# Kernel optimization log

Hardware: AMD Instinct MI355X
Metric: run time of the kernel (lower is better)

The kernel has to match this reference:

```python
import jax, jax.numpy as jnp
import numpy as np

DG = 8            # deformable_groups
MAX_RES = 10.0    # max_residual_magnitude
K = 9             # 3x3 kernel positions


def conv3(x, w, b):
    y = jax.lax.conv_general_dilated(x, w, (1, 1), [(1, 1), (1, 1)],
                                     dimension_numbers=('NCHW', 'OIHW', 'NCHW'))
    return y + b[None, :, None, None]


def lrelu(v):
    return jnp.where(v >= 0, v, 0.1 * v)


def deform_conv2d(x, offset, mask, weight, bias):
    # x: [B,C,H,W]; offset: [B,2*DG*K,H,W] (per group, K points, (y,x) interleaved)
    # mask: [B,DG*K,H,W]; weight: [O,C,3,3]; stride=1, pad=1, dil=1, groups=1
    B, C, H, W = x.shape
    Cg = C // DG
    off = offset.reshape(B, DG, K, 2, H, W)
    dtype = x.dtype
    dy = (jnp.arange(K) // 3 - 1).astype(dtype)
    dx = (jnp.arange(K) % 3 - 1).astype(dtype)
    py = off[:, :, :, 0] + jnp.arange(H, dtype=dtype)[None, None, None, :, None] + dy[None, None, :, None, None]
    px = off[:, :, :, 1] + jnp.arange(W, dtype=dtype)[None, None, None, None, :] + dx[None, None, :, None, None]
    y0 = jnp.floor(py)
    x0 = jnp.floor(px)
    x_flat = x.reshape(B, DG, Cg, H * W)
    m = mask.reshape(B, DG, K, H, W)
    acc = jnp.zeros((B, DG, Cg, K, H, W), dtype=dtype)
    for iy, wy in ((y0, y0 + 1.0 - py), (y0 + 1.0, py - y0)):
        for ix, wx in ((x0, x0 + 1.0 - px), (x0 + 1.0, px - x0)):
            valid = (iy >= 0) & (iy < H) & (ix >= 0) & (ix < W)
            yi = jnp.clip(iy, 0, H - 1).astype(jnp.int32)
            xi = jnp.clip(ix, 0, W - 1).astype(jnp.int32)
            idx = (yi * W + xi).reshape(B, DG, 1, K * H * W)
            g = jnp.take_along_axis(x_flat, idx, axis=3).reshape(B, DG, Cg, K, H, W)
            wgt = (wy * wx * valid.astype(dtype) * m)[:, :, None]  # mask folded in
            acc = acc + g * wgt
    O = weight.shape[0]
    out = jnp.einsum('bgckhw,ogck->bohw', acc, weight.reshape(O, DG, Cg, K))
    return out + bias[None, :, None, None]


def setup_inputs() -> dict:
    key = jax.random.key(0)
    ks = jax.random.split(key, 12)
    B, C, H, W = 4, 64, 128, 128
    inp = {
        'x': jax.random.normal(ks[0], (B, C, H, W), jnp.float32),
        'x_warped0': jax.random.normal(ks[1], (B, C, H, W), jnp.float32),
        'x_current': jax.random.normal(ks[2], (B, C, H, W), jnp.float32),
        'flow0': jax.random.normal(ks[3], (B, 2, H, W), jnp.float32),
        'w1': jax.random.normal(ks[4], (64, 130, 3, 3), jnp.float32) * 0.05,
        'b1': jnp.zeros((64,), jnp.float32),
        'w2': jax.random.normal(ks[5], (64, 64, 3, 3), jnp.float32) * 0.05,
        'b2': jnp.zeros((64,), jnp.float32),
        'w3': jax.random.normal(ks[6], (64, 64, 3, 3), jnp.float32) * 0.05,
        'b3': jnp.zeros((64,), jnp.float32),
        'w4': jax.random.normal(ks[7], (216, 64, 3, 3), jnp.float32) * 0.05,
        'b4': jnp.zeros((216,), jnp.float32),
        'weight': jax.random.normal(ks[8], (64, 64, 3, 3), jnp.float32) * 0.05,
        'bias': jnp.zeros((64,), jnp.float32),
    }
    return inp


def reference(x, x_warped0, x_current, flow0, w1, b1, w2, b2, w3, b3, w4, b4, weight, bias):
    # conv_offset stack on cat([x_warped0, x_current, flow0])
    feat = jnp.concatenate([x_warped0, x_current, flow0], axis=1)  # [B, 2C+2, H, W]
    o = lrelu(conv3(feat, w1, b1))
    o = lrelu(conv3(o, w2, b2))
    o = lrelu(conv3(o, w3, b3))
    o = conv3(o, w4, b4)  # [B, 3*K*DG, H, W]
    out1, out2, mask = jnp.split(o, 3, axis=1)
    offset = MAX_RES * jnp.tanh(jnp.concatenate([out1, out2], axis=1))  # [B, 2*K*DG, H, W]
    # flows[0].flip(1).repeat(1, K*DG, 1, 1): (y,x) flow tiled over all sample points
    offset = offset + jnp.tile(flow0[:, ::-1], (1, K * DG, 1, 1))
    mask = jax.nn.sigmoid(mask)
    return deform_conv2d(x, offset, mask, weight, bias)
```

## Files before the change

### kernel.cpp

```cpp
#include <hip/hip_runtime.h>
#include <math.h>

#define HH 128
#define WW 128
#define BB 4
#define HW (HH*WW)

typedef unsigned short u16;
typedef unsigned int u32;
typedef __bf16 bf16x8 __attribute__((ext_vector_type(8)));
typedef float f32x4 __attribute__((ext_vector_type(4)));

__device__ __forceinline__ u16 f2bf(float x) {
    u32 u = __float_as_uint(x);
    return (u16)((u + 0x7fffu + ((u >> 16) & 1u)) >> 16);
}
__device__ __forceinline__ float bf2f(u16 h) {
    return __uint_as_float(((u32)h) << 16);
}
__device__ __forceinline__ bf16x8 ld8(const u16* p) {
    union { uint4 u; bf16x8 v; } c;
    c.u = *(const uint4*)p;
    return c.v;
}
__device__ __forceinline__ bf16x8 cvt8(uint4 u) {
    union { uint4 u; bf16x8 v; } c;
    c.u = u;
    return c.v;
}

__global__ void split_w_k(const float* __restrict__ src, u16* __restrict__ dh,
                          u16* __restrict__ dl, int OC, int OCpad, int CIN, int CINpad)
{
    const int i = blockIdx.x * 256 + threadIdx.x;
    const int tot = OCpad * 9 * CINpad;
    if (i >= tot) return;
    const int oc = i / (9 * CINpad);
    const int r = i - oc * 9 * CINpad;
    const int tap = r / CINpad;
    const int cin = r - tap * CINpad;
    float v = 0.f;
    if (oc < OC && cin < CIN) v = src[((size_t)oc * CIN + cin) * 9 + tap];
    const u16 h = f2bf(v);
    dh[i] = h;
    dl[i] = f2bf(v - bf2f(h));
}

__global__ void pad_bias_k(const float* __restrict__ b, float* __restrict__ bp)
{
    const int i = blockIdx.x * 256 + threadIdx.x;
    if (i < 256) bp[i] = (i < 216) ? b[i] : 0.f;
}

__global__ void pack_dw_k(const float* __restrict__ wt, u16* __restrict__ Apack)
{
    const int i = blockIdx.x * 256 + threadIdx.x;
    if (i >= 36864) return;
    const int jj = i & 7;
    const int fr = (i >> 3) & 15;
    const int m  = (i >> 7) & 3;
    const int fq = (i >> 9) & 3;
    const int kk = i >> 11;
    const int oc = m * 16 + fr;
    const int j  = kk * 32 + fq * 8 + jj;
    const int tap = j >> 3, c = j & 7;
    const int g = tap / 9, kt = tap - g * 9;
    const int ch = g * 8 + c;
    Apack[i] = f2bf(wt[((size_t)oc * 64 + ch) * 9 + kt]);
}

template<int CREC>
__global__ __launch_bounds__(256) void pack_x_k(
    const float* __restrict__ A, const float* __restrict__ B2,
    const float* __restrict__ C3, u16* __restrict__ dst)
{
    const int i = blockIdx.x * 256 + threadIdx.x;
    const int b = i >> 14;
    const int px = i & 16383;
    u16* rec = dst + (size_t)i * (CREC * 2);

#pragma unroll
    for (int g = 0; g < CREC / 32; ++g) {
#pragma unroll
        for (int cb = 0; cb < 4; ++cb) {
            u32 hwv[4], lwv[4];
#pragma unroll
            for (int p = 0; p < 4; ++p) {
                float v[2];
#pragma unroll
                for (int e = 0; e < 2; ++e) {
                    const int c = g * 32 + cb * 8 + p * 2 + e;
                    float vv;
                    if (c < 64)       vv = A[((size_t)(b * 64 + c)) * HW + px];
                    else if (c < 128) vv = B2[((size_t)(b * 64 + c - 64)) * HW + px];
                    else if (c < 130) vv = C3[((size_t)(b * 2 + c - 128)) * HW + px];
                    else              vv = 0.f;
                    v[e] = vv;
                }
                const u16 h0 = f2bf(v[0]), h1 = f2bf(v[1]);
                const u16 l0 = f2bf(v[0] - bf2f(h0)), l1 = f2bf(v[1] - bf2f(h1));
                hwv[p] = (u32)h0 | ((u32)h1 << 16);
                lwv[p] = (u32)l0 | ((u32)l1 << 16);
            }
            uint4 H; H.x = hwv[0]; H.y = hwv[1]; H.z = hwv[2]; H.w = hwv[3];
            uint4 L; L.x = lwv[0]; L.y = lwv[1]; L.z = lwv[2]; L.w = lwv[3];
            *(uint4*)(rec + g * 64 + cb * 16)     = H;
            *(uint4*)(rec + g * 64 + cb * 16 + 8) = L;
        }
    }
}

template<int NCHUNK, int KGLAST, int MODE, bool RELU, bool PACKOUT, int MINW, int NJ>
__global__ __launch_bounds__(256, MINW) void conv_pk_k(
    const u16* __restrict__ Xp, const u16* __restrict__ Wh, const u16* __restrict__ Wl,
    const float* __restrict__ bias, float* __restrict__ outf, u16* __restrict__ outp,
    int OCreal)
{
    const int ROWS = 4;
    const int NPX = (ROWS + 2) * 18;
    __shared__ u16 Xs[NPX * 136];
    const int CINpad = (NCHUNK - 1) * 64 + KGLAST * 32;
    const int CRECU16 = CINpad * 2;

    const int tile = blockIdx.x;
    const int h0 = (tile >> 3) * ROWS;
    const int w0 = (tile & 7) * 16;
    const int b = blockIdx.z;
    const int t = threadIdx.x;
    const int lane = t & 63, wv = t >> 6;
    const int fr = lane & 15, fq = lane >> 4;

    const int mbase = (MODE == 1) ? (wv * NJ) : 0;

    f32x4 acc0[4];
    f32x4 acc1[NJ][4];
    if (MODE == 0) {
        const float4 bv = *(const float4*)(bias + wv * 16 + 4 * fq);
#pragma unroll
        for (int n = 0; n < 4; ++n) {
            acc0[n][0] = bv.x; acc0[n][1] = bv.y; acc0[n][2] = bv.z; acc0[n][3] = bv.w;
        }
    } else {
#pragma unroll
        for (int m = 0; m < NJ; ++m) {
            const float4 bv = *(const float4*)(bias + (mbase + m) * 16 + 4 * fq);
#pragma unroll
            for (int n = 0; n < 4; ++n) {
                acc1[m][n][0] = bv.x; acc1[m][n][1] = bv.y;
                acc1[m][n][2] = bv.z; acc1[m][n][3] = bv.w;
            }
        }
    }

    const u16* WhL = Wh + (size_t)fr * 9 * CINpad + 8 * fq;
    const u16* WlL = Wl + (size_t)fr * 9 * CINpad + 8 * fq;

#pragma unroll
    for (int chunk = 0; chunk < NCHUNK; ++chunk) {
        const int nkg = (chunk == NCHUNK - 1) ? KGLAST : 2;
        const int nu = nkg * 8;
        __syncthreads();
        for (int s = t; s < NPX * nu; s += 256) {
            const int px = s / nu, o = s - px * nu;
            const int hy = px / 18, hx = px - hy * 18;
            const int gy = h0 + hy - 1, gx = w0 + hx - 1;
            uint4 v; v.x = 0; v.y = 0; v.z = 0; v.w = 0;
            if (gy >= 0 && gy < HH && gx >= 0 && gx < WW)
                v = *(const uint4*)(Xp + ((size_t)(b * HW + gy * WW + gx)) * CRECU16
                                       + chunk * 128 + o * 8);
            *(uint4*)(Xs + px * 136 + o * 8) = v;
        }
        __syncthreads();

        if (MODE == 0) {
#pragma unroll
            for (int tap = 0; tap < 9; ++tap) {
                const int ky = tap / 3, kx = tap % 3;
#pragma unroll
                for (int kg = 0; kg < 2; ++kg) {
                    if (kg >= nkg) break;
                    const size_t off = (size_t)(wv * 144 + tap) * CINpad + chunk * 64 + kg * 32;
                    const bf16x8 Ah = ld8(WhL + off);
                    const bf16x8 Al = ld8(WlL + off);
#pragma unroll
                    for (int n = 0; n < 4; ++n) {
                        const int hp = (n + ky) * 18 + fr + kx;
                        const u16* Bp = Xs + hp * 136 + kg * 64 + fq * 16;
                        const bf16x8 Bh = ld8(Bp);
                        const bf16x8 Bl = ld8(Bp + 8);
                        acc0[n] = __builtin_amdgcn_mfma_f32_16x16x32_bf16(Ah, Bh, acc0[n], 0, 0, 0);
                        acc0[n] = __builtin_amdgcn_mfma_f32_16x16x32_bf16(Ah, Bl, acc0[n], 0, 0, 0);
                        acc0[n] = __builtin_amdgcn_mfma_f32_16x16x32_bf16(Al, Bh, acc0[n], 0, 0, 0);
                    }
                }
            }
        } else {
            auto PF = [&](int tap, bf16x8 (&Dh)[2 * NJ], bf16x8 (&Dl)[2 * NJ]) {
#pragma unroll
                for (int kg = 0; kg < 2; ++kg)
#pragma unroll
                    for (int m = 0; m < NJ; ++m) {
                        const size_t off = (size_t)((mbase + m) * 144 + tap) * CINpad
                                         + chunk * 64 + kg * 32;
                        Dh[kg * NJ + m] = ld8(WhL + off);
                        Dl[kg * NJ + m] = ld8(WlL + off);
                    }
            };
            auto CMP = [&](int tap, bf16x8 (&Dh)[2 * NJ], bf16x8 (&Dl)[2 * NJ]) {
                const int ky = tap / 3, kx = tap - 3 * ky;
#pragma unroll
                for (int kg = 0; kg < 2; ++kg) {
#pragma unroll
                    for (int n = 0; n < 4; ++n) {
                        const int hp = (n + ky) * 18 + fr + kx;
                        const u16* Bp = Xs + hp * 136 + kg * 64 + fq * 16;
                        const bf16x8 Bh = ld8(Bp);
                        const bf16x8 Bl = ld8(Bp + 8);
#pragma unroll
                        for (int m = 0; m < NJ; ++m) {
                            acc1[m][n] = __builtin_amdgcn_mfma_f32_16x16x32_bf16(Dh[kg * NJ + m], Bh, acc1[m][n], 0, 0, 0);
                            acc1[m][n] = __builtin_amdgcn_mfma_f32_16x16x32_bf16(Dh[kg * NJ + m], Bl, acc1[m][n], 0, 0, 0);
                            acc1[m][n] = __builtin_amdgcn_mfma_f32_16x16x32_bf16(Dl[kg * NJ + m], Bh, acc1[m][n], 0, 0, 0);
                        }
                    }
                }
            };

            bf16x8 PaH[2 * NJ], PaL[2 * NJ], PbH[2 * NJ], PbL[2 * NJ];
            PF(0, PaH, PaL);
#pragma unroll 1
            for (int tp = 0; tp < 4; ++tp) {
                PF(2 * tp + 1, PbH, PbL);
                CMP(2 * tp, PaH, PaL);
                PF(2 * tp + 2, PaH, PaL);
                CMP(2 * tp + 1, PbH, PbL);
            }
            CMP(8, PaH, PaL);
        }
    }

    if (MODE == 1) {
#pragma unroll
        for (int m = 0; m < NJ; ++m) {
            const int mt = mbase + m;
#pragma unroll
            for (int n = 0; n < 4; ++n)
#pragma unroll
                for (int i = 0; i < 4; ++i) {
                    const int oc = mt * 16 + 4 * fq + i;
                    if (oc < OCreal) {
                        float v = acc1[m][n][i];
                        if (mt < 9) {
                            const float a = fabsf(v);
                            const float e = __expf(-2.f * a);
                            float tv = (1.f - e) * __builtin_amdgcn_rcpf(1.f + e);
                            v = 10.f * copysignf(tv, v);
                        } else {
                            v = __builtin_amdgcn_rcpf(1.f + __expf(-v));
                        }
                        outf[((size_t)(b * OCreal + oc)) * HW + (h0 + n) * WW + w0 + fr] = v;
                    }
                }
        }
    } else if (!PACKOUT) {
#pragma unroll
        for (int n = 0; n < 4; ++n)
#pragma unroll
            for (int i = 0; i < 4; ++i) {
                const int oc = wv * 16 + 4 * fq + i;
                if (oc < OCreal) {
                    float v = acc0[n][i];
                    if (RELU) v = (v >= 0.f) ? v : 0.1f * v;
                    outf[((size_t)(b * OCreal + oc)) * HW + (h0 + n) * WW + w0 + fr] = v;
                }
            }
    } else {
        __syncthreads();
        const int coff = (wv >> 1) * 64 + (((wv << 1) + (fq >> 1)) & 3) * 16 + ((fq & 1) << 2);
#pragma unroll
        for (int n = 0; n < 4; ++n) {
            u16 hh[4], ll[4];
#pragma unroll
            for (int i = 0; i < 4; ++i) {
                float v = acc0[n][i];
                if (RELU) v = (v >= 0.f) ? v : 0.1f * v;
                hh[i] = f2bf(v);
                ll[i] = f2bf(v - bf2f(hh[i]));
            }
            uint2 H, L;
            H.x = (u32)hh[0] | ((u32)hh[1] << 16);
            H.y = (u32)hh[2] | ((u32)hh[3] << 16);
            L.x = (u32)ll[0] | ((u32)ll[1] << 16);
            L.y = (u32)ll[2] | ((u32)ll[3] << 16);
            const int pxe = n * 16 + fr;
            u16* E = Xs + pxe * 136 + coff;
            *(uint2*)E = H;
            *(uint2*)(E + 8) = L;
        }
        __syncthreads();
        for (int i = t; i < 1024; i += 256) {
            const int px = i >> 4, o = i & 15;
            const uint4 v = *(const uint4*)(Xs + px * 136 + o * 8);
            const int gp = (h0 + (px >> 4)) * WW + w0 + (px & 15);
            *(uint4*)(outp + ((size_t)(b * HW + gp)) * 128 + o * 8) = v;
        }
    }
}

__global__ __launch_bounds__(256) void pack_xb_k(
    const float* __restrict__ x, uint4* __restrict__ xqb)
{
    const int i = blockIdx.x * 256 + threadIdx.x;
    const int pix = i & (HW - 1);
    const int g = (i >> 14) & 7;
    const int b = i >> 17;
    const float* xp = x + ((size_t)(b * 64 + g * 8)) * HW + pix;
    u32 w[4];
#pragma unroll
    for (int c2 = 0; c2 < 4; ++c2) {
        const u16 l = f2bf(xp[(size_t)(2 * c2) * HW]);
        const u16 h = f2bf(xp[(size_t)(2 * c2 + 1) * HW]);
        w[c2] = (u32)l | ((u32)h << 16);
    }
    uint4 v; v.x = w[0]; v.y = w[1]; v.z = w[2]; v.w = w[3];
    xqb[(size_t)(b * 8 + g) * HW + pix] = v;
}

__device__ __forceinline__ unsigned pk_bf16(float lo, float hi) {
    unsigned a = __float_as_uint(lo), b = __float_as_uint(hi);
    return ((a + 0x8000u) >> 16) | ((b + 0x8000u) & 0xffff0000u);
}

__global__ __launch_bounds__(512, 8) void deform_fused_k(
    const uint4* __restrict__ xqb, const float* __restrict__ o4,
    const float* __restrict__ flow, const uint4* __restrict__ Apack,
    const float* __restrict__ bias, float* __restrict__ out)
{
    __shared__ u16 sv[32 * 584];

    const int bid0 = blockIdx.x;
    const int bid = (bid0 & 7) * 256 + (bid0 >> 3);
    const int b = bid >> 9;
    const int pix0 = (bid & 511) << 5;
    const int t = threadIdx.x;

    {
        const int gpx = t & 31;
        const int g = (t >> 5) & 7;
        const int kh = t >> 8;
        const int kbase = kh * 4;
        const int pix = pix0 + gpx;
        const int h = pix >> 7, w = pix & (WW - 1);
        const float fy = flow[((size_t)b * 2 + 1) * HW + pix];
        const float fx = flow[((size_t)b * 2 + 0) * HW + pix];
        const float* ob = o4 + (size_t)b * 216 * HW + pix;
        const uint4* qg = xqb + (size_t)(b * 8 + g) * HW;

        int   code[5];
        float w00[5], w01[5], w10[5], w11[5];

#pragma unroll
        for (int j = 0; j < 5; ++j) {
            if (j == 4 && !kh) break;
            const int k = kbase + j;
            const float oy = ob[(size_t)(g * 18 + k * 2) * HW];
            const float ox = ob[(size_t)(g * 18 + k * 2 + 1) * HW];
            const float mm = ob[(size_t)(144 + g * 9 + k) * HW];

            const float ppy = oy + fy + (float)(h + k / 3 - 1);
            const float ppx = ox + fx + (float)(w + k % 3 - 1);

            const float y0f = floorf(ppy), x0f = floorf(ppx);
            const float ly = ppy - y0f, lx = ppx - x0f;
            const int iy0 = (int)y0f, ix0 = (int)x0f;
            const int iy1 = iy0 + 1,  ix1 = ix0 + 1;

            const float vy0 = (iy0 >= 0 && iy0 < HH) ? 1.f : 0.f;
            const float vy1 = (iy1 >= 0 && iy1 < HH) ? 1.f : 0.f;
            const float vx0 = (ix0 >= 0 && ix0 < WW) ? 1.f : 0.f;
            const float vx1 = (ix1 >= 0 && ix1 < WW) ? 1.f : 0.f;

            const int cy0 = min(max(iy0, 0), HH - 1);
            const int cy1 = min(max(iy1, 0), HH - 1);
            const int cx0 = min(max(ix0, 0), WW - 1);
            const int cx1 = min(max(ix1, 0), WW - 1);

            w00[j] = (1.f - ly) * (1.f - lx) * vy0 * vx0 * mm;
            w01[j] = (1.f - ly) * lx         * vy0 * vx1 * mm;
            w10[j] = ly         * (1.f - lx) * vy1 * vx0 * mm;
            w11[j] = ly         * lx         * vy1 * vx1 * mm;

            code[j] = (cy0 * WW + cx0) | ((cx1 - cx0) << 14) | ((cy1 - cy0) << 15);
        }

        u16* svp = sv + gpx * 584 + g * 72 + kbase * 8;
#pragma unroll
        for (int j = 0; j < 5; ++j) {
            if (j == 4 && !kh) break;
            const int i00 = code[j] & 16383;
            const int i01 = i00 + ((code[j] >> 14) & 1);
            const int i10 = i00 + (((code[j] >> 15) & 1) << 7);
            const int i11 = i10 + ((code[j] >> 14) & 1);

            const uint4 A4 = qg[i00];
            const uint4 B4 = qg[i01];
            const uint4 C4 = qg[i10];
            const uint4 D4 = qg[i11];
            const float W00 = w00[j], W01 = w01[j], W10 = w10[j], W11 = w11[j];

            uint4 P;
            u32 pw[4];
#pragma unroll
            for (int c2 = 0; c2 < 4; ++c2) {
                const u32 aw = (&A4.x)[c2], bw = (&B4.x)[c2];
                const u32 cw = (&C4.x)[c2], dw = (&D4.x)[c2];
                const float alo = __uint_as_float(aw << 16), ahi = __uint_as_float(aw & 0xffff0000u);
                const float blo = __uint_as_float(bw << 16), bhi = __uint_as_float(bw & 0xffff0000u);
                const float clo = __uint_as_float(cw << 16), chi = __uint_as_float(cw & 0xffff0000u);
                const float dlo = __uint_as_float(dw << 16), dhi = __uint_as_float(dw & 0xffff0000u);
                const float slo = W00 * alo + W01 * blo + W10 * clo + W11 * dlo;
                const float shi = W00 * ahi + W01 * bhi + W10 * chi + W11 * dhi;
                pw[c2] = pk_bf16(slo, shi);
            }
            P.x = pw[0]; P.y = pw[1]; P.z = pw[2]; P.w = pw[3];
            *(uint4*)(svp + (size_t)j * 8) = P;
        }
    }
    __syncthreads();

    {
        const int lane = t & 63, wv = t >> 6;
        const int mt = wv & 3, nt = wv >> 2;
        const int fr = lane & 15, fq = lane >> 4;

        f32x4 acc;
        acc[0] = 0.f; acc[1] = 0.f; acc[2] = 0.f; acc[3] = 0.f;

#pragma unroll
        for (int kk = 0; kk < 18; ++kk) {
            const bf16x8 A = cvt8(Apack[((kk * 4 + fq) * 4 + mt) * 16 + fr]);
            const bf16x8 Bf = ld8(sv + (size_t)(nt * 16 + fr) * 584 + kk * 32 + fq * 8);
            acc = __builtin_amdgcn_mfma_f32_16x16x32_bf16(A, Bf, acc, 0, 0, 0);
        }

        const float4 bv = *(const float4*)(bias + mt * 16 + 4 * fq);
        const float bb[4] = { bv.x, bv.y, bv.z, bv.w };
        const int pix = pix0 + nt * 16 + fr;
#pragma unroll
        for (int i = 0; i < 4; ++i) {
            const int oc = mt * 16 + 4 * fq + i;
            out[((size_t)b * 64 + oc) * HW + pix] = acc[i] + bb[i];
        }
    }
}

extern "C" void kernel_launch(void* const* d_in, const int* in_sizes, int n_in,
                              void* d_out, int out_size, void* d_ws, size_t ws_size,
                              hipStream_t stream)
{
    const float* x     = (const float*)d_in[0];
    const float* xw    = (const float*)d_in[1];
    const float* xc    = (const float*)d_in[2];
    const float* flow  = (const float*)d_in[3];
    const float* w1    = (const float*)d_in[4];
    const float* b1    = (const float*)d_in[5];
    const float* w2    = (const float*)d_in[6];
    const float* b2    = (const float*)d_in[7];
    const float* w3    = (const float*)d_in[8];
    const float* b3    = (const float*)d_in[9];
    const float* w4    = (const float*)d_in[10];
    const float* b4    = (const float*)d_in[11];
    const float* wt    = (const float*)d_in[12];
    const float* bias  = (const float*)d_in[13];
    float* out = (float*)d_out;

    char* ws = (char*)d_ws;
    u16*   X1p  = (u16*)(ws);
    float* o4   = (float*)(ws);
    u16*   buf1 = (u16*)(ws + 56623104);
    u16*   buf2 = (u16*)(ws + 73400320);
    u16* Apack = (u16*)(ws + 90177536);
    u16* W1h = (u16*)(ws + 90251264);
    u16* W1l = (u16*)(ws + 90435584);
    u16* W2h = (u16*)(ws + 90619904);
    u16* W2l = (u16*)(ws + 90693632);
    u16* W3h = (u16*)(ws + 90767360);
    u16* W3l = (u16*)(ws + 90841088);
    u16* W4h = (u16*)(ws + 90914816);
    u16* W4l = (u16*)(ws + 91209728);
    float* b4p = (float*)(ws + 91504640);

    const dim3 blk(256);

    split_w_k<<<dim3((64 * 9 * 160 + 255) / 256), blk, 0, stream>>>(w1, W1h, W1l, 64, 64, 130, 160);
    split_w_k<<<dim3((64 * 9 * 64 + 255) / 256), blk, 0, stream>>>(w2, W2h, W2l, 64, 64, 64, 64);
    split_w_k<<<dim3((64 * 9 * 64 + 255) / 256), blk, 0, stream>>>(w3, W3h, W3l, 64, 64, 64, 64);
    split_w_k<<<dim3((256 * 9 * 64 + 255) / 256), blk, 0, stream>>>(w4, W4h, W4l, 216, 256, 64, 64);
    pad_bias_k<<<dim3(1), blk, 0, stream>>>(b4, b4p);
    pack_dw_k<<<dim3(144), blk, 0, stream>>>(wt, Apack);

    pack_x_k<160><<<dim3(BB * HW / 256), blk, 0, stream>>>(xw, xc, flow, X1p);
    conv_pk_k<3, 1, 0, true, true, 2, 4><<<dim3(256, 1, BB), blk, 0, stream>>>(
        X1p, W1h, W1l, b1, nullptr, buf1, 64);
    conv_pk_k<1, 2, 0, true, true, 2, 4><<<dim3(256, 1, BB), blk, 0, stream>>>(
        buf1, W2h, W2l, b2, nullptr, buf2, 64);
    conv_pk_k<1, 2, 0, true, true, 2, 4><<<dim3(256, 1, BB), blk, 0, stream>>>(
        buf2, W3h, W3l, b3, nullptr, buf1, 64);
    pack_xb_k<<<dim3(BB * 8 * HW / 256), blk, 0, stream>>>(x, (uint4*)buf2);
    conv_pk_k<1, 2, 1, false, false, 1, 4><<<dim3(256, 1, BB), blk, 0, stream>>>(
        buf1, W4h, W4l, b4p, o4, nullptr, 216);

    deform_fused_k<<<dim3(BB * HW / 32), dim3(512), 0, stream>>>(
        (const uint4*)buf2, o4, flow, (const uint4*)Apack, bias, out);
}
```

Measured before the change: 285.4 us.

## Retile offset/mask conv into 8-row tiles split across channel halves

```diff
diff --git a/kernel.cpp b/kernel.cpp
--- a/kernel.cpp
+++ b/kernel.cpp
@@ -116,7 +116,7 @@
     const float* __restrict__ bias, float* __restrict__ outf, u16* __restrict__ outp,
     int OCreal)
 {
-    const int ROWS = 4;
+    const int ROWS = (MODE == 1) ? 8 : 4;
     const int NPX = (ROWS + 2) * 18;
     __shared__ u16 Xs[NPX * 136];
     const int CINpad = (NCHUNK - 1) * 64 + KGLAST * 32;
@@ -130,7 +130,8 @@
     const int lane = t & 63, wv = t >> 6;
     const int fr = lane & 15, fq = lane >> 4;
 
-    const int mbase = (MODE == 1) ? (wv * NJ) : 0;
+    const int mg = wv >> 1, rg = wv & 1;
+    const int mbase = (MODE == 1) ? (blockIdx.y * 8 + mg * NJ) : 0;
 
     f32x4 acc0[4];
     f32x4 acc1[NJ][4];
@@ -195,47 +196,46 @@
                 }
             }
         } else {
-            auto PF = [&](int tap, bf16x8 (&Dh)[2 * NJ], bf16x8 (&Dl)[2 * NJ]) {
-#pragma unroll
-                for (int kg = 0; kg < 2; ++kg)
+            auto PF = [&](int s, bf16x8 (&Dh)[NJ], bf16x8 (&Dl)[NJ]) {
+                const int tap = s >> 1, kg = s & 1;
+#pragma unroll
+                for (int m = 0; m < NJ; ++m) {
+                    const size_t off = (size_t)((mbase + m) * 144 + tap) * CINpad
+                                     + chunk * 64 + kg * 32;
+                    Dh[m] = ld8(WhL + off);
+                    Dl[m] = ld8(WlL + off);
+                }
+            };
+            auto CMP = [&](int s, bf16x8 (&Dh)[NJ], bf16x8 (&Dl)[NJ]) {
+                const int tap = s >> 1, kg = s & 1;
+                const int ky = tap / 3, kx = tap - 3 * ky;
+#pragma unroll
+                for (int n = 0; n < 4; ++n) {
+                    const int hp = (rg * 4 + n + ky) * 18 + fr + kx;
+                    const u16* Bp = Xs + hp * 136 + kg * 64 + fq * 16;
+                    const bf16x8 Bh = ld8(Bp);
+                    const bf16x8 Bl = ld8(Bp + 8);
 #pragma unroll
                     for (int m = 0; m < NJ; ++m) {
-                        const size_t off = (size_t)((mbase + m) * 144 + tap) * CINpad
-                                         + chunk * 64 + kg * 32;
-                        Dh[kg * NJ + m] = ld8(WhL + off);
-                        Dl[kg * NJ + m] = ld8(WlL + off);
-                    }
-            };
-            auto CMP = [&](int tap, bf16x8 (&Dh)[2 * NJ], bf16x8 (&Dl)[2 * NJ]) {
-                const int ky = tap / 3, kx = tap - 3 * ky;
-#pragma unroll
-                for (int kg = 0; kg < 2; ++kg) {
-#pragma unroll
-                    for (int n = 0; n < 4; ++n) {
-                        const int hp = (n + ky) * 18 + fr + kx;
-                        const u16* Bp = Xs + hp * 136 + kg * 64 + fq * 16;
-                        const bf16x8 Bh = ld8(Bp);
-                        const bf16x8 Bl = ld8(Bp + 8);
-#pragma unroll
-                        for (int m = 0; m < NJ; ++m) {
-                            acc1[m][n] = __builtin_amdgcn_mfma_f32_16x16x32_bf16(Dh[kg * NJ + m], Bh, acc1[m][n], 0, 0, 0);
-                            acc1[m][n] = __builtin_amdgcn_mfma_f32_16x16x32_bf16(Dh[kg * NJ + m], Bl, acc1[m][n], 0, 0, 0);
-                            acc1[m][n] = __builtin_amdgcn_mfma_f32_16x16x32_bf16(Dl[kg * NJ + m], Bh, acc1[m][n], 0, 0, 0);
-                        }
+                        acc1[m][n] = __builtin_amdgcn_mfma_f32_16x16x32_bf16(Dh[m], Bh, acc1[m][n], 0, 0, 0);
+                        acc1[m][n] = __builtin_amdgcn_mfma_f32_16x16x32_bf16(Dh[m], Bl, acc1[m][n], 0, 0, 0);
+                        acc1[m][n] = __builtin_amdgcn_mfma_f32_16x16x32_bf16(Dl[m], Bh, acc1[m][n], 0, 0, 0);
                     }
                 }
             };
 
-            bf16x8 PaH[2 * NJ], PaL[2 * NJ], PbH[2 * NJ], PbL[2 * NJ];
+            bf16x8 PaH[NJ], PaL[NJ], PbH[NJ], PbL[NJ];
             PF(0, PaH, PaL);
 #pragma unroll 1
-            for (int tp = 0; tp < 4; ++tp) {
-                PF(2 * tp + 1, PbH, PbL);
-                CMP(2 * tp, PaH, PaL);
-                PF(2 * tp + 2, PaH, PaL);
-                CMP(2 * tp + 1, PbH, PbL);
-            }
-            CMP(8, PaH, PaL);
+            for (int sp = 0; sp < 8; ++sp) {
+                PF(2 * sp + 1, PbH, PbL);
+                CMP(2 * sp, PaH, PaL);
+                PF(2 * sp + 2, PaH, PaL);
+                CMP(2 * sp + 1, PbH, PbL);
+            }
+            PF(17, PbH, PbL);
+            CMP(16, PaH, PaL);
+            CMP(17, PbH, PbL);
         }
     }
 
@@ -258,7 +258,7 @@
                         } else {
                             v = __builtin_amdgcn_rcpf(1.f + __expf(-v));
                         }
-                        outf[((size_t)(b * OCreal + oc)) * HW + (h0 + n) * WW + w0 + fr] = v;
+                        outf[((size_t)(b * OCreal + oc)) * HW + (h0 + rg * 4 + n) * WW + w0 + fr] = v;
                     }
                 }
         }
@@ -507,7 +507,7 @@
     conv_pk_k<1, 2, 0, true, true, 2, 4><<<dim3(256, 1, BB), blk, 0, stream>>>(
         buf2, W3h, W3l, b3, nullptr, buf1, 64);
     pack_xb_k<<<dim3(BB * 8 * HW / 256), blk, 0, stream>>>(x, (uint4*)buf2);
-    conv_pk_k<1, 2, 1, false, false, 1, 4><<<dim3(256, 1, BB), blk, 0, stream>>>(
+    conv_pk_k<1, 2, 1, false, false, 1, 4><<<dim3(128, 2, BB), blk, 0, stream>>>(
         buf1, W4h, W4l, b4p, o4, nullptr, 216);
 
     deform_fused_k<<<dim3(BB * HW / 32), dim3(512), 0, stream>>>(
```

Measured after the change: 289.8 us. Within noise of the previous version (+1.5%).
